# Optimization experiments

Hardware: AMD Instinct MI355X
Metric: run time of the kernel (lower is better)

## Reference

```python
import jax, jax.numpy as jnp
import numpy as np

NPG = 100          # nodes per graph
NUM_GRAPHS = 500
N = NPG * NUM_GRAPHS
DEG = 32
E = N * DEG
IN_DIM = 100
HID = 64           # out_channels / hidden_dim
HEADS = 2
NCLS = 2


def setup_inputs() -> dict:
    key = jax.random.key(0)
    ks = jax.random.split(key, 24)
    rng = np.random.default_rng(0)
    # edges within each graph, guaranteed no self-loops
    dst = np.repeat(np.arange(N), DEG)
    off = rng.integers(1, NPG, size=E)
    src = (dst // NPG) * NPG + ((dst % NPG) + off) % NPG
    edge_index = jnp.asarray(np.stack([src, dst]).astype(np.int32))
    batch = jnp.asarray((np.arange(N) // NPG).astype(np.int32))
    HC = HEADS * HID
    p = lambda k, sh: jax.random.normal(k, sh, jnp.float32) * 0.1
    return dict(
        x=jax.random.normal(ks[0], (N, IN_DIM), jnp.float32),
        edge_attr=jax.random.uniform(ks[1], (E,), jnp.float32),
        W1=p(ks[2], (IN_DIM, HC)), as1=p(ks[3], (HEADS, HID)), ad1=p(ks[4], (HEADS, HID)), bg1=p(ks[5], (HC,)),
        l1W=p(ks[6], (HC, HID)), l1b=p(ks[7], (HID,)), g1=jnp.ones((HID,), jnp.float32), b1=jnp.zeros((HID,), jnp.float32),
        W2=p(ks[8], (HID, HC)), as2=p(ks[9], (HEADS, HID)), ad2=p(ks[10], (HEADS, HID)), bg2=p(ks[11], (HC,)),
        l2W=p(ks[12], (HC, HID)), l2b=p(ks[13], (HID,)), g2=jnp.ones((HID,), jnp.float32), b2=jnp.zeros((HID,), jnp.float32),
        f1W=p(ks[14], (HID, HID)), f1b=p(ks[15], (HID,)),
        f2W=p(ks[16], (HID, HID // 2)), f2b=p(ks[17], (HID // 2,)),
        f3W=p(ks[18], (HID // 2, NCLS)), f3b=p(ks[19], (NCLS,)),
        edge_index=edge_index, batch=batch)


def reference(x, edge_attr, W1, as1, ad1, bg1, l1W, l1b, g1, b1,
              W2, as2, ad2, bg2, l2W, l2b, g2, b2,
              f1W, f1b, f2W, f2b, f3W, f3b, edge_index, batch):
    n = x.shape[0]
    ea = jnp.abs(edge_attr)  # computed as in forward; unused by attention_weighted variant
    # GATConv adds self-loops (fill doesn't matter for alpha-only message)
    sl = jnp.arange(n, dtype=edge_index.dtype)
    src = jnp.concatenate([edge_index[0], sl])
    dst = jnp.concatenate([edge_index[1], sl])
    lrelu = lambda z: jax.nn.leaky_relu(z, 0.2)

    def gat(h, W, a_s, a_d, bias):
        xp = (h @ W).reshape(n, HEADS, HID)                 # [N,H,C]
        e = lrelu(jnp.sum(xp * a_s, -1)[src] + jnp.sum(xp * a_d, -1)[dst])  # [E',H]
        m = jax.ops.segment_max(e, dst, num_segments=n)
        ex = jnp.exp(e - m[dst])
        alpha = ex / jax.ops.segment_sum(ex, dst, num_segments=n)[dst]      # edge softmax per dst
        out = jax.ops.segment_sum(xp[src] * alpha[:, :, None], dst, num_segments=n)
        return out.reshape(n, HEADS * HID) + bias

    def bn(z, g, b):  # BatchNorm1d with batch statistics (biased var, eps=1e-5)
        return (z - z.mean(0)) * jax.lax.rsqrt(z.var(0) + 1e-5) * g + b

    z = bn(lrelu(gat(x, W1, as1, ad1, bg1) @ l1W + l1b), g1, b1)
    z = bn(lrelu(gat(z, W2, as2, ad2, bg2) @ l2W + l2b), g2, b2)
    # global mean pool
    s = jax.ops.segment_sum(z, batch, num_segments=NUM_GRAPHS)
    cnt = jax.ops.segment_sum(jnp.ones((n, 1), z.dtype), batch, num_segments=NUM_GRAPHS)
    z = s / cnt
    z = lrelu(z @ f1W + f1b)
    z = lrelu(z @ f2W + f2b)
    return z @ f3W + f3b
```

## Files before the change

### kernel.cpp

```cpp
#include <hip/hip_runtime.h>

#define NN 50000
#define NPGc 100
#define NG 500
#define DEG 32
#define HC 128
#define HID 64

__device__ __forceinline__ float lrelu(float x) { return x > 0.0f ? x : 0.2f * x; }

__global__ void k_prep(const float* __restrict__ W, const float* __restrict__ as_,
                       const float* __restrict__ ad_, float* __restrict__ Wext, int K) {
  int t = threadIdx.x;
  for (int u = t; u < K * 128; u += blockDim.x) {
    int k = u >> 7, c = u & 127;
    Wext[k * 132 + c] = W[u];
  }
  for (int u = t; u < K * 4; u += blockDim.x) {
    int k = u >> 2, s = u & 3;
    const float* a = (s < 2) ? as_ : ad_;
    int h = s & 1;
    float acc = 0.f;
    for (int c = 0; c < 64; ++c) acc += W[k * 128 + h * 64 + c] * a[h * 64 + c];
    Wext[k * 132 + 128 + s] = acc;
  }
}

template <int K, bool BN>
__global__ __launch_bounds__(256) void k_in_gemm(
    const float* __restrict__ in, const float* __restrict__ Wext,
    const float* __restrict__ AB, float* __restrict__ xp,
    float* __restrict__ ssrc, float* __restrict__ sdst) {
  constexpr int KP = (K % 8 == 0) ? K + 4 : K;
  __shared__ __align__(16) float xs[64 * KP];
  __shared__ __align__(16) float wl[K * 132];
  int t = threadIdx.x;
  int n0 = blockIdx.x * 64;

  for (int u = t; u < K * 33; u += 256) ((float4*)wl)[u] = ((const float4*)Wext)[u];

  constexpr int RQ = K / 4;
  for (int u = t; u < 64 * RQ; u += 256) {
    int r = u / RQ, q = u % RQ;
    int n = n0 + r;
    float4 v = make_float4(0.f, 0.f, 0.f, 0.f);
    if (n < NN) v = ((const float4*)(in + (size_t)n * K))[q];
    if (BN) {
      float4 a4 = ((const float4*)AB)[q];
      float4 b4 = ((const float4*)(AB + 64))[q];
      v.x = v.x * a4.x + b4.x; v.y = v.y * a4.y + b4.y;
      v.z = v.z * a4.z + b4.z; v.w = v.w * a4.w + b4.w;
    }
    ((float4*)(xs + r * KP))[q] = v;
  }
  __syncthreads();

  int ng = t >> 5, cg = t & 31;
  int r0 = ng * 8;
  float4 acc[8];
#pragma unroll
  for (int i = 0; i < 8; ++i) acc[i] = make_float4(0.f, 0.f, 0.f, 0.f);

  for (int k = 0; k < K; ++k) {
    float4 w4 = ((float4*)wl)[k * 33 + cg];
#pragma unroll
    for (int i = 0; i < 8; ++i) {
      float a = xs[(r0 + i) * KP + k];
      acc[i].x += a * w4.x; acc[i].y += a * w4.y;
      acc[i].z += a * w4.z; acc[i].w += a * w4.w;
    }
  }
#pragma unroll
  for (int i = 0; i < 8; ++i) {
    int n = n0 + r0 + i;
    if (n < NN) ((float4*)(xp + (size_t)n * HC))[cg] = acc[i];
  }
  {
    int r = t >> 2, s = t & 3;
    float sc = 0.f;
    for (int k = 0; k < K; ++k) sc += xs[r * KP + k] * wl[k * 132 + 128 + s];
    int n = n0 + r;
    if (n < NN) {
      if (s < 2) ssrc[n * 2 + s] = sc;
      else       sdst[n * 2 + (s - 2)] = sc;
    }
  }
}

__global__ __launch_bounds__(256) void k_gat(
    const float* __restrict__ xp, const float* __restrict__ ssrc,
    const float* __restrict__ sdst, const int* __restrict__ esrc,
    const float* __restrict__ bg, float* __restrict__ out) {
  __shared__ __align__(16) float xl[NPGc * HC];
  __shared__ float ssl[NPGc * 2];
  __shared__ float sdl[NPGc * 2];
  __shared__ unsigned short srcl[NPGc * DEG];
  __shared__ float alpha[NPGc * 2 * (DEG + 2)];
  int t = threadIdx.x;
  int base = blockIdx.x * NPGc;

  for (int u = t; u < NPGc * (HC / 4); u += 256)
    ((float4*)xl)[u] = ((const float4*)(xp + (size_t)base * HC))[u];
  for (int u = t; u < NPGc * 2; u += 256) {
    ssl[u] = ssrc[base * 2 + u];
    sdl[u] = sdst[base * 2 + u];
  }
  for (int u = t; u < NPGc * DEG; u += 256)
    srcl[u] = (unsigned short)(esrc[base * DEG + u] - base);
  __syncthreads();

  if (t < NPGc * 2) {
    int d = t >> 1, h = t & 1;
    float sd = sdl[d * 2 + h];
    float es = lrelu(ssl[d * 2 + h] + sd);
    float m = es;
    float e[DEG];
#pragma unroll
    for (int j = 0; j < DEG; ++j) {
      int s = srcl[d * DEG + j];
      e[j] = lrelu(ssl[s * 2 + h] + sd);
      m = fmaxf(m, e[j]);
    }
    float exs = __expf(es - m);
    float den = exs;
#pragma unroll
    for (int j = 0; j < DEG; ++j) { e[j] = __expf(e[j] - m); den += e[j]; }
    float inv = 1.0f / den;
    float* al = alpha + (d * 2 + h) * (DEG + 2);
#pragma unroll
    for (int j = 0; j < DEG; ++j) al[j] = e[j] * inv;
    al[DEG] = exs * inv;
  }
  __syncthreads();

  for (int u = t; u < NPGc * 32; u += 256) {
    int d = u >> 5, c4 = u & 31, h = c4 >> 4;
    const float* al = alpha + (d * 2 + h) * (DEG + 2);
    const unsigned short* sp = srcl + d * DEG;
    float aself = al[DEG];
    float4 x4 = ((float4*)xl)[d * 32 + c4];
    float4 acc;
    acc.x = aself * x4.x; acc.y = aself * x4.y;
    acc.z = aself * x4.z; acc.w = aself * x4.w;
#pragma unroll 8
    for (int j = 0; j < DEG; ++j) {
      float a = al[j];
      float4 v = ((float4*)xl)[(int)sp[j] * 32 + c4];
      acc.x += a * v.x; acc.y += a * v.y;
      acc.z += a * v.z; acc.w += a * v.w;
    }
    float4 bgv = ((const float4*)bg)[c4];
    acc.x += bgv.x; acc.y += bgv.y; acc.z += bgv.z; acc.w += bgv.w;
    ((float4*)(out + (size_t)(base + d) * HC))[c4] = acc;
  }
}

__global__ __launch_bounds__(256) void k_out_gemm(
    const float* __restrict__ gin, const float* __restrict__ lW,
    const float* __restrict__ lb, float* __restrict__ h,
    float* __restrict__ partial) {
  __shared__ __align__(16) float gl[64 * 132];
  __shared__ __align__(16) float wl[HC * HID];
  __shared__ float psum[2 * HID];
  int t = threadIdx.x;
  int n0 = blockIdx.x * 64;

  for (int u = t; u < 64 * 32; u += 256) {
    int r = u >> 5, q = u & 31;
    int n = n0 + r;
    float4 v = make_float4(0.f, 0.f, 0.f, 0.f);
    if (n < NN) v = ((const float4*)(gin + (size_t)n * HC))[q];
    ((float4*)(gl + r * 132))[q] = v;
  }
  for (int u = t; u < HC * (HID / 4); u += 256)
    ((float4*)wl)[u] = ((const float4*)lW)[u];
  if (t < 2 * HID) psum[t] = 0.f;
  __syncthreads();

  int ng = t >> 4, cg = t & 15;
  int r0 = ng * 4;
  float4 acc[4];
#pragma unroll
  for (int i = 0; i < 4; ++i) acc[i] = make_float4(0.f, 0.f, 0.f, 0.f);

  for (int k = 0; k < HC; ++k) {
    float4 w4 = ((float4*)wl)[k * 16 + cg];
#pragma unroll
    for (int i = 0; i < 4; ++i) {
      float a = gl[(r0 + i) * 132 + k];
      acc[i].x += a * w4.x; acc[i].y += a * w4.y;
      acc[i].z += a * w4.z; acc[i].w += a * w4.w;
    }
  }
  float4 bias = ((const float4*)lb)[cg];
  float s0 = 0, s1 = 0, s2 = 0, s3 = 0, q0 = 0, q1 = 0, q2 = 0, q3 = 0;
#pragma unroll
  for (int i = 0; i < 4; ++i) {
    int n = n0 + r0 + i;
    if (n < NN) {
      float4 v;
      v.x = lrelu(acc[i].x + bias.x); v.y = lrelu(acc[i].y + bias.y);
      v.z = lrelu(acc[i].z + bias.z); v.w = lrelu(acc[i].w + bias.w);
      ((float4*)(h + (size_t)n * HID))[cg] = v;
      s0 += v.x; q0 += v.x * v.x; s1 += v.y; q1 += v.y * v.y;
      s2 += v.z; q2 += v.z * v.z; s3 += v.w; q3 += v.w * v.w;
    }
  }
  int c0 = cg * 4;
  atomicAdd(&psum[c0 + 0], s0); atomicAdd(&psum[c0 + 1], s1);
  atomicAdd(&psum[c0 + 2], s2); atomicAdd(&psum[c0 + 3], s3);
  atomicAdd(&psum[HID + c0 + 0], q0); atomicAdd(&psum[HID + c0 + 1], q1);
  atomicAdd(&psum[HID + c0 + 2], q2); atomicAdd(&psum[HID + c0 + 3], q3);
  __syncthreads();
  if (t < 2 * HID) partial[blockIdx.x * 128 + t] = psum[t];
}

__global__ __launch_bounds__(256) void k_stats(
    const float* __restrict__ partial, int nb, const float* __restrict__ gamma,
    const float* __restrict__ beta, float* __restrict__ AB) {
  __shared__ float red[2][256];
  int c = blockIdx.x, t = threadIdx.x;
  float s = 0.f, sq = 0.f;
  for (int i = t; i < nb; i += 256) {
    s += partial[i * 128 + c];
    sq += partial[i * 128 + 64 + c];
  }
  red[0][t] = s; red[1][t] = sq;
  __syncthreads();
  for (int o = 128; o > 0; o >>= 1) {
    if (t < o) { red[0][t] += red[0][t + o]; red[1][t] += red[1][t + o]; }
    __syncthreads();
  }
  if (t == 0) {
    float mean = red[0][0] / (float)NN;
    float var = red[1][0] / (float)NN - mean * mean;
    float A = gamma[c] * rsqrtf(var + 1e-5f);
    AB[c] = A;
    AB[64 + c] = beta[c] - mean * A;
  }
}

__global__ __launch_bounds__(64) void k_pool_mlp(
    const float* __restrict__ h2, const float* __restrict__ AB,
    const float* __restrict__ f1W, const float* __restrict__ f1b,
    const float* __restrict__ f2W, const float* __restrict__ f2b,
    const float* __restrict__ f3W, const float* __restrict__ f3b,
    float* __restrict__ out) {
  __shared__ float pooled[64];
  __shared__ float z1[64];
  __shared__ float z2[32];
  int g = blockIdx.x, t = threadIdx.x;
  const float* hb = h2 + (size_t)g * NPGc * HID;
  float s = 0.f;
  for (int r = 0; r < NPGc; ++r) s += hb[r * HID + t];
  pooled[t] = (s * (1.0f / NPGc)) * AB[t] + AB[64 + t];
  __syncthreads();
  float a = f1b[t];
  for (int c = 0; c < 64; ++c) a += pooled[c] * f1W[c * 64 + t];
  z1[t] = lrelu(a);
  __syncthreads();
  if (t < 32) {
    float a2 = f2b[t];
    for (int c = 0; c < 64; ++c) a2 += z1[c] * f2W[c * 32 + t];
    z2[t] = lrelu(a2);
  }
  __syncthreads();
  if (t < 2) {
    float a3 = f3b[t];
    for (int c = 0; c < 32; ++c) a3 += z2[c] * f3W[c * 2 + t];
    out[g * 2 + t] = a3;
  }
}

extern "C" void kernel_launch(void* const* d_in, const int* in_sizes, int n_in,
                              void* d_out, int out_size, void* d_ws, size_t ws_size,
                              hipStream_t stream) {
  const float* x   = (const float*)d_in[0];
  const float* W1  = (const float*)d_in[2];
  const float* as1 = (const float*)d_in[3];
  const float* ad1 = (const float*)d_in[4];
  const float* bg1 = (const float*)d_in[5];
  const float* l1W = (const float*)d_in[6];
  const float* l1b = (const float*)d_in[7];
  const float* g1  = (const float*)d_in[8];
  const float* b1  = (const float*)d_in[9];
  const float* W2  = (const float*)d_in[10];
  const float* as2 = (const float*)d_in[11];
  const float* ad2 = (const float*)d_in[12];
  const float* bg2 = (const float*)d_in[13];
  const float* l2W = (const float*)d_in[14];
  const float* l2b = (const float*)d_in[15];
  const float* g2  = (const float*)d_in[16];
  const float* b2  = (const float*)d_in[17];
  const float* f1W = (const float*)d_in[18];
  const float* f1b = (const float*)d_in[19];
  const float* f2W = (const float*)d_in[20];
  const float* f2b = (const float*)d_in[21];
  const float* f3W = (const float*)d_in[22];
  const float* f3b = (const float*)d_in[23];
  const int* esrc  = (const int*)d_in[24];
  float* out = (float*)d_out;

  float* ws = (float*)d_ws;
  size_t off = 0;
  auto alloc = [&](size_t nf) { float* p = ws + off; off += (nf + 63) & ~(size_t)63; return p; };
  float* Wext1   = alloc(100 * 132);
  float* Wext2   = alloc(64 * 132);
  float* xp      = alloc((size_t)NN * HC);
  float* ssrc    = alloc((size_t)NN * 2);
  float* sdst    = alloc((size_t)NN * 2);
  float* gout    = alloc((size_t)NN * HC);
  float* hbuf    = alloc((size_t)NN * HID);
  const int NB = (NN + 63) / 64;
  float* partial = alloc((size_t)NB * 128);
  float* AB1     = alloc(128);
  float* AB2     = alloc(128);
  (void)in_sizes; (void)n_in; (void)out_size; (void)ws_size;

  k_prep<<<1, 256, 0, stream>>>(W1, as1, ad1, Wext1, 100);
  k_prep<<<1, 256, 0, stream>>>(W2, as2, ad2, Wext2, 64);
  k_in_gemm<100, false><<<NB, 256, 0, stream>>>(x, Wext1, nullptr, xp, ssrc, sdst);
  k_gat<<<NG, 256, 0, stream>>>(xp, ssrc, sdst, esrc, bg1, gout);
  k_out_gemm<<<NB, 256, 0, stream>>>(gout, l1W, l1b, hbuf, partial);
  k_stats<<<64, 256, 0, stream>>>(partial, NB, g1, b1, AB1);
  k_in_gemm<64, true><<<NB, 256, 0, stream>>>(hbuf, Wext2, AB1, xp, ssrc, sdst);
  k_gat<<<NG, 256, 0, stream>>>(xp, ssrc, sdst, esrc, bg2, gout);
  k_out_gemm<<<NB, 256, 0, stream>>>(gout, l2W, l2b, hbuf, partial);
  k_stats<<<64, 256, 0, stream>>>(partial, NB, g2, b2, AB2);
  k_pool_mlp<<<NG, 64, 0, stream>>>(hbuf, AB2, f1W, f1b, f2W, f2b, f3W, f3b, out);
}
```

Baseline: 351.8 us.

## Split GAT per head, read GEMM weights from global, parallelize pooling

```diff
diff --git a/kernel.cpp b/kernel.cpp
--- a/kernel.cpp
+++ b/kernel.cpp
@@ -9,35 +9,35 @@
 
 __device__ __forceinline__ float lrelu(float x) { return x > 0.0f ? x : 0.2f * x; }
 
-__global__ void k_prep(const float* __restrict__ W, const float* __restrict__ as_,
-                       const float* __restrict__ ad_, float* __restrict__ Wext, int K) {
+__global__ void k_prep(const float* __restrict__ W1, const float* __restrict__ as1,
+                       const float* __restrict__ ad1, float* __restrict__ Wa1,
+                       const float* __restrict__ W2, const float* __restrict__ as2,
+                       const float* __restrict__ ad2, float* __restrict__ Wa2) {
+  const float* W  = blockIdx.x ? W2 : W1;
+  const float* as_ = blockIdx.x ? as2 : as1;
+  const float* ad_ = blockIdx.x ? ad2 : ad1;
+  float* Wa = blockIdx.x ? Wa2 : Wa1;
+  int K = blockIdx.x ? 64 : 100;
   int t = threadIdx.x;
-  for (int u = t; u < K * 128; u += blockDim.x) {
-    int k = u >> 7, c = u & 127;
-    Wext[k * 132 + c] = W[u];
-  }
   for (int u = t; u < K * 4; u += blockDim.x) {
     int k = u >> 2, s = u & 3;
     const float* a = (s < 2) ? as_ : ad_;
     int h = s & 1;
     float acc = 0.f;
     for (int c = 0; c < 64; ++c) acc += W[k * 128 + h * 64 + c] * a[h * 64 + c];
-    Wext[k * 132 + 128 + s] = acc;
+    Wa[k * 4 + s] = acc;
   }
 }
 
 template <int K, bool BN>
 __global__ __launch_bounds__(256) void k_in_gemm(
-    const float* __restrict__ in, const float* __restrict__ Wext,
-    const float* __restrict__ AB, float* __restrict__ xp,
-    float* __restrict__ ssrc, float* __restrict__ sdst) {
+    const float* __restrict__ in, const float* __restrict__ W,
+    const float* __restrict__ Wa, const float* __restrict__ AB,
+    float* __restrict__ xp, float* __restrict__ ssrc, float* __restrict__ sdst) {
   constexpr int KP = (K % 8 == 0) ? K + 4 : K;
   __shared__ __align__(16) float xs[64 * KP];
-  __shared__ __align__(16) float wl[K * 132];
   int t = threadIdx.x;
   int n0 = blockIdx.x * 64;
-
-  for (int u = t; u < K * 33; u += 256) ((float4*)wl)[u] = ((const float4*)Wext)[u];
 
   constexpr int RQ = K / 4;
   for (int u = t; u < 64 * RQ; u += 256) {
@@ -61,13 +61,16 @@
 #pragma unroll
   for (int i = 0; i < 8; ++i) acc[i] = make_float4(0.f, 0.f, 0.f, 0.f);
 
+  const float4* W4 = (const float4*)W;
+  float4 w4 = W4[cg];
   for (int k = 0; k < K; ++k) {
-    float4 w4 = ((float4*)wl)[k * 33 + cg];
+    float4 wc = w4;
+    if (k + 1 < K) w4 = W4[(k + 1) * 32 + cg];
 #pragma unroll
     for (int i = 0; i < 8; ++i) {
       float a = xs[(r0 + i) * KP + k];
-      acc[i].x += a * w4.x; acc[i].y += a * w4.y;
-      acc[i].z += a * w4.z; acc[i].w += a * w4.w;
+      acc[i].x += a * wc.x; acc[i].y += a * wc.y;
+      acc[i].z += a * wc.z; acc[i].w += a * wc.w;
     }
   }
 #pragma unroll
@@ -78,7 +81,7 @@
   {
     int r = t >> 2, s = t & 3;
     float sc = 0.f;
-    for (int k = 0; k < K; ++k) sc += xs[r * KP + k] * wl[k * 132 + 128 + s];
+    for (int k = 0; k < K; ++k) sc += xs[r * KP + k] * Wa[k * 4 + s];
     int n = n0 + r;
     if (n < NN) {
       if (s < 2) ssrc[n * 2 + s] = sc;
@@ -91,34 +94,34 @@
     const float* __restrict__ xp, const float* __restrict__ ssrc,
     const float* __restrict__ sdst, const int* __restrict__ esrc,
     const float* __restrict__ bg, float* __restrict__ out) {
-  __shared__ __align__(16) float xl[NPGc * HC];
-  __shared__ float ssl[NPGc * 2];
-  __shared__ float sdl[NPGc * 2];
+  __shared__ __align__(16) float xl[NPGc * 64];
+  __shared__ float sh[NPGc];
+  __shared__ float sdh[NPGc];
   __shared__ unsigned short srcl[NPGc * DEG];
-  __shared__ float alpha[NPGc * 2 * (DEG + 2)];
+  __shared__ float alpha[NPGc * (DEG + 2)];
   int t = threadIdx.x;
-  int base = blockIdx.x * NPGc;
-
-  for (int u = t; u < NPGc * (HC / 4); u += 256)
-    ((float4*)xl)[u] = ((const float4*)(xp + (size_t)base * HC))[u];
-  for (int u = t; u < NPGc * 2; u += 256) {
-    ssl[u] = ssrc[base * 2 + u];
-    sdl[u] = sdst[base * 2 + u];
+  int g = blockIdx.x >> 1, h = blockIdx.x & 1;
+  int base = g * NPGc;
+
+  const float4* xp4 = (const float4*)(xp + (size_t)base * HC);
+  for (int u = t; u < NPGc * 16; u += 256)
+    ((float4*)xl)[u] = xp4[(u >> 4) * 32 + h * 16 + (u & 15)];
+  if (t < NPGc) {
+    sh[t] = ssrc[(base + t) * 2 + h];
+    sdh[t] = sdst[(base + t) * 2 + h];
   }
   for (int u = t; u < NPGc * DEG; u += 256)
     srcl[u] = (unsigned short)(esrc[base * DEG + u] - base);
   __syncthreads();
 
-  if (t < NPGc * 2) {
-    int d = t >> 1, h = t & 1;
-    float sd = sdl[d * 2 + h];
-    float es = lrelu(ssl[d * 2 + h] + sd);
+  if (t < NPGc) {
+    float sd = sdh[t];
+    float es = lrelu(sh[t] + sd);
     float m = es;
     float e[DEG];
 #pragma unroll
     for (int j = 0; j < DEG; ++j) {
-      int s = srcl[d * DEG + j];
-      e[j] = lrelu(ssl[s * 2 + h] + sd);
+      e[j] = lrelu(sh[srcl[t * DEG + j]] + sd);
       m = fmaxf(m, e[j]);
     }
     float exs = __expf(es - m);
@@ -126,32 +129,32 @@
 #pragma unroll
     for (int j = 0; j < DEG; ++j) { e[j] = __expf(e[j] - m); den += e[j]; }
     float inv = 1.0f / den;
-    float* al = alpha + (d * 2 + h) * (DEG + 2);
+    float* al = alpha + t * (DEG + 2);
 #pragma unroll
     for (int j = 0; j < DEG; ++j) al[j] = e[j] * inv;
     al[DEG] = exs * inv;
   }
   __syncthreads();
 
-  for (int u = t; u < NPGc * 32; u += 256) {
-    int d = u >> 5, c4 = u & 31, h = c4 >> 4;
-    const float* al = alpha + (d * 2 + h) * (DEG + 2);
+  int c4 = t & 15;
+  float4 bgv = ((const float4*)bg)[h * 16 + c4];
+  for (int d = t >> 4; d < NPGc; d += 16) {
+    const float* al = alpha + d * (DEG + 2);
     const unsigned short* sp = srcl + d * DEG;
     float aself = al[DEG];
-    float4 x4 = ((float4*)xl)[d * 32 + c4];
+    float4 x4 = ((float4*)xl)[d * 16 + c4];
     float4 acc;
     acc.x = aself * x4.x; acc.y = aself * x4.y;
     acc.z = aself * x4.z; acc.w = aself * x4.w;
 #pragma unroll 8
     for (int j = 0; j < DEG; ++j) {
       float a = al[j];
-      float4 v = ((float4*)xl)[(int)sp[j] * 32 + c4];
+      float4 v = ((float4*)xl)[(int)sp[j] * 16 + c4];
       acc.x += a * v.x; acc.y += a * v.y;
       acc.z += a * v.z; acc.w += a * v.w;
     }
-    float4 bgv = ((const float4*)bg)[c4];
     acc.x += bgv.x; acc.y += bgv.y; acc.z += bgv.z; acc.w += bgv.w;
-    ((float4*)(out + (size_t)(base + d) * HC))[c4] = acc;
+    ((float4*)out)[(size_t)(base + d) * 32 + h * 16 + c4] = acc;
   }
 }
 
@@ -160,7 +163,6 @@
     const float* __restrict__ lb, float* __restrict__ h,
     float* __restrict__ partial) {
   __shared__ __align__(16) float gl[64 * 132];
-  __shared__ __align__(16) float wl[HC * HID];
   __shared__ float psum[2 * HID];
   int t = threadIdx.x;
   int n0 = blockIdx.x * 64;
@@ -172,8 +174,6 @@
     if (n < NN) v = ((const float4*)(gin + (size_t)n * HC))[q];
     ((float4*)(gl + r * 132))[q] = v;
   }
-  for (int u = t; u < HC * (HID / 4); u += 256)
-    ((float4*)wl)[u] = ((const float4*)lW)[u];
   if (t < 2 * HID) psum[t] = 0.f;
   __syncthreads();
 
@@ -183,13 +183,16 @@
 #pragma unroll
   for (int i = 0; i < 4; ++i) acc[i] = make_float4(0.f, 0.f, 0.f, 0.f);
 
+  const float4* lW4 = (const float4*)lW;
+  float4 w4 = lW4[cg];
   for (int k = 0; k < HC; ++k) {
-    float4 w4 = ((float4*)wl)[k * 16 + cg];
+    float4 wc = w4;
+    if (k + 1 < HC) w4 = lW4[(k + 1) * 16 + cg];
 #pragma unroll
     for (int i = 0; i < 4; ++i) {
       float a = gl[(r0 + i) * 132 + k];
-      acc[i].x += a * w4.x; acc[i].y += a * w4.y;
-      acc[i].z += a * w4.z; acc[i].w += a * w4.w;
+      acc[i].x += a * wc.x; acc[i].y += a * wc.y;
+      acc[i].z += a * wc.z; acc[i].w += a * wc.w;
     }
   }
   float4 bias = ((const float4*)lb)[cg];
@@ -246,14 +249,21 @@
     const float* __restrict__ f2W, const float* __restrict__ f2b,
     const float* __restrict__ f3W, const float* __restrict__ f3b,
     float* __restrict__ out) {
+  __shared__ float pp[4 * 64];
   __shared__ float pooled[64];
   __shared__ float z1[64];
   __shared__ float z2[32];
   int g = blockIdx.x, t = threadIdx.x;
-  const float* hb = h2 + (size_t)g * NPGc * HID;
-  float s = 0.f;
-  for (int r = 0; r < NPGc; ++r) s += hb[r * HID + t];
-  pooled[t] = (s * (1.0f / NPGc)) * AB[t] + AB[64 + t];
+  const float4* hb4 = (const float4*)(h2 + (size_t)g * NPGc * HID);
+  int rq = t >> 4, c4 = t & 15;
+  float4 s4 = make_float4(0.f, 0.f, 0.f, 0.f);
+  for (int r = rq; r < NPGc; r += 4) {
+    float4 v = hb4[r * 16 + c4];
+    s4.x += v.x; s4.y += v.y; s4.z += v.z; s4.w += v.w;
+  }
+  ((float4*)pp)[rq * 16 + c4] = s4;
+  __syncthreads();
+  pooled[t] = (pp[t] + pp[64 + t] + pp[128 + t] + pp[192 + t]) * (1.0f / NPGc) * AB[t] + AB[64 + t];
   __syncthreads();
   float a = f1b[t];
   for (int c = 0; c < 64; ++c) a += pooled[c] * f1W[c * 64 + t];
@@ -304,8 +314,8 @@
   float* ws = (float*)d_ws;
   size_t off = 0;
   auto alloc = [&](size_t nf) { float* p = ws + off; off += (nf + 63) & ~(size_t)63; return p; };
-  float* Wext1   = alloc(100 * 132);
-  float* Wext2   = alloc(64 * 132);
+  float* Wa1     = alloc(100 * 4);
+  float* Wa2     = alloc(64 * 4);
   float* xp      = alloc((size_t)NN * HC);
   float* ssrc    = alloc((size_t)NN * 2);
   float* sdst    = alloc((size_t)NN * 2);
@@ -317,14 +327,13 @@
   float* AB2     = alloc(128);
   (void)in_sizes; (void)n_in; (void)out_size; (void)ws_size;
 
-  k_prep<<<1, 256, 0, stream>>>(W1, as1, ad1, Wext1, 100);
-  k_prep<<<1, 256, 0, stream>>>(W2, as2, ad2, Wext2, 64);
-  k_in_gemm<100, false><<<NB, 256, 0, stream>>>(x, Wext1, nullptr, xp, ssrc, sdst);
-  k_gat<<<NG, 256, 0, stream>>>(xp, ssrc, sdst, esrc, bg1, gout);
+  k_prep<<<2, 256, 0, stream>>>(W1, as1, ad1, Wa1, W2, as2, ad2, Wa2);
+  k_in_gemm<100, false><<<NB, 256, 0, stream>>>(x, W1, Wa1, nullptr, xp, ssrc, sdst);
+  k_gat<<<NG * 2, 256, 0, stream>>>(xp, ssrc, sdst, esrc, bg1, gout);
   k_out_gemm<<<NB, 256, 0, stream>>>(gout, l1W, l1b, hbuf, partial);
   k_stats<<<64, 256, 0, stream>>>(partial, NB, g1, b1, AB1);
-  k_in_gemm<64, true><<<NB, 256, 0, stream>>>(hbuf, Wext2, AB1, xp, ssrc, sdst);
-  k_gat<<<NG, 256, 0, stream>>>(xp, ssrc, sdst, esrc, bg2, gout);
+  k_in_gemm<64, true><<<NB, 256, 0, stream>>>(hbuf, W2, Wa2, AB1, xp, ssrc, sdst);
+  k_gat<<<NG * 2, 256, 0, stream>>>(xp, ssrc, sdst, esrc, bg2, gout);
   k_out_gemm<<<NB, 256, 0, stream>>>(gout, l2W, l2b, hbuf, partial);
   k_stats<<<64, 256, 0, stream>>>(partial, NB, g2, b2, AB2);
   k_pool_mlp<<<NG, 64, 0, stream>>>(hbuf, AB2, f1W, f1b, f2W, f2b, f3W, f3b, out);
```

After: 320.7 us. 1.1x faster.
